# Optimization experiments

Hardware: AMD Instinct MI355X
Metric: run time of the kernel (lower is better)

Reference implementation:

```python
import jax, jax.numpy as jnp
import numpy as np

DIM = 512
HEADS = 8
HEAD_DIM = DIM // HEADS
SCALE = HEAD_DIM ** -0.5
LN_EPS = 1e-5


def _layernorm(t, g, b):
    mu = jnp.mean(t, axis=-1, keepdims=True)
    var = jnp.mean(jnp.square(t - mu), axis=-1, keepdims=True)
    return (t - mu) * jax.lax.rsqrt(var + LN_EPS) * g + b


def setup_inputs() -> dict:
    key = jax.random.key(0)
    ks = jax.random.split(key, 8)
    B, C, H, W = 2, DIM, 48, 48
    s = 1.0 / np.sqrt(DIM)
    return {
        "x": jax.random.normal(ks[0], (B, C, H, W), jnp.float32),
        "y": jax.random.normal(ks[1], (B, C, H, W), jnp.float32),
        # linear weights stored [in, out]
        "k_w": jax.random.uniform(ks[2], (DIM, DIM), jnp.float32, -s, s),
        "k_b": jax.random.uniform(ks[3], (DIM,), jnp.float32, -s, s),
        "qv_w": jax.random.uniform(ks[4], (DIM, 2 * DIM), jnp.float32, -s, s),
        "qv_b": jax.random.uniform(ks[5], (2 * DIM,), jnp.float32, -s, s),
        "lnx_g": jnp.ones((DIM,), jnp.float32),
        "lnx_b": jnp.zeros((DIM,), jnp.float32),
        "lny_g": jnp.ones((DIM,), jnp.float32),
        "lny_b": jnp.zeros((DIM,), jnp.float32),
    }


def _split_qv(t, qv_w, qv_b):
    B, N, C = t.shape
    qv = (t @ qv_w + qv_b).reshape(B, N, 2, HEADS, HEAD_DIM)
    qv = jnp.transpose(qv, (2, 0, 3, 1, 4))  # [2, B, h, N, d]
    return qv[0], qv[1]


def _heads(t):
    B, N, C = t.shape
    return jnp.transpose(t.reshape(B, N, HEADS, HEAD_DIM), (0, 2, 1, 3))  # [B,h,N,d]


def reference(x, y, k_w, k_b, qv_w, qv_b, lnx_g, lnx_b, lny_g, lny_b):
    B, C = x.shape[0], x.shape[1]
    xf = _layernorm(jnp.transpose(x.reshape(B, C, -1), (0, 2, 1)), lnx_g, lnx_b)  # [B,N,C]
    yf = _layernorm(jnp.transpose(y.reshape(B, C, -1), (0, 2, 1)), lny_g, lny_b)
    N = xf.shape[1]

    y_q, y_v = _split_qv(yf, qv_w, qv_b)
    x_q, x_v = _split_qv(xf, qv_w, qv_b)
    y_k = _heads(yf @ k_w + k_b)
    x_k = _heads(xf @ k_w + k_b)

    # branch 1: softmax(x_q y_k^T) x_v  -> standard [B,N,C]
    a1 = jax.nn.softmax(jnp.einsum('bhnd,bhmd->bhnm', x_q, y_k) * SCALE, axis=-1)
    xo = jnp.einsum('bhnm,bhmd->bhnd', a1, x_v)
    xo = jnp.transpose(xo, (0, 2, 1, 3)).reshape(B, N, C)

    # branch 2: faithful reproduction of torch quirk (x_k kept a leading 1-dim,
    # so the output [1,B,h,N,d].transpose(1,2).reshape(B,N,C) scrambles layout)
    a2 = jax.nn.softmax(jnp.einsum('bhnd,bhmd->bhnm', y_q, x_k) * SCALE, axis=-1)
    yo = jnp.einsum('bhnm,bhmd->bhnd', a2, y_v)  # [B,h,N,d]
    yo = jnp.transpose(yo[None], (0, 2, 1, 3, 4)).reshape(B, N, C)

    return jnp.concatenate([xo, yo], axis=0)  # [2B, N, C]
```

## Files before the change

### kernel.cpp

```cpp
#include <hip/hip_runtime.h>

#define DIM 512
#define NTOK 2304
#define HEADS 8
#define HD 64
#define LN_EPS 1e-5f
#define BNC 2359296
#define QSC 0.18033688011112042f

typedef __attribute__((ext_vector_type(8))) short short8;
typedef __attribute__((ext_vector_type(4))) short sh4;
typedef __attribute__((ext_vector_type(4))) float f32x4;

__device__ __forceinline__ short f2bf(float f) {
    union { float f; unsigned u; } x; x.f = f;
    unsigned r = (x.u + 0x7fffu + ((x.u >> 16) & 1u)) >> 16;
    return (short)(r & 0xffffu);
}
__device__ __forceinline__ unsigned fbits(float f) {
    union { float f; unsigned u; } x; x.f = f; return x.u;
}
__device__ __forceinline__ void gl2lds(const short* g, short* l) {
    __builtin_amdgcn_global_load_lds(
        (const __attribute__((address_space(1))) unsigned int*)g,
        (__attribute__((address_space(3))) unsigned int*)l, 16, 0, 0);
}

__global__ void k_prep(const float* __restrict__ x, const float* __restrict__ y,
                       float* __restrict__ mu, float* __restrict__ rs,
                       const float* __restrict__ qv_w, const float* __restrict__ k_w,
                       const float* __restrict__ qv_b, const float* __restrict__ k_b,
                       short* __restrict__ Wt, float* __restrict__ bias) {
    __shared__ __align__(16) float tile[64][65];
    int bx = blockIdx.x, tid = threadIdx.x;
    if (bx < 36) {
        int id = bx * 256 + tid;
        int n = id % NTOK;
        int sb = id / NTOK;
        int s = sb >> 1, b = sb & 1;
        const float* src = (s ? y : x) + (size_t)b * DIM * NTOK + n;
        float sum = 0.f, sq = 0.f;
        for (int c = 0; c < DIM; c++) {
            float v = src[(size_t)c * NTOK];
            sum += v; sq += v * v;
        }
        float m = sum * (1.0f / DIM);
        float var = sq * (1.0f / DIM) - m * m;
        mu[id] = m;
        rs[id] = rsqrtf(var + LN_EPS);
        return;
    }
    int idx = bx - 36;
    int jt = idx % 24, ct = idx / 24;
    int j0 = jt * 64, c0 = ct * 64;
    if (ct == 0 && tid < 64) {
        int j = j0 + tid;
        bias[j] = (j < 1024) ? qv_b[j] : k_b[j - 1024];
    }
    for (int slot = tid; slot < 1024; slot += 256) {
        int r = slot >> 4, q = slot & 15;
        int c = c0 + r;
        float4 v;
        if (j0 < 1024) v = *(const float4*)(qv_w + (size_t)c * 1024 + j0 + q * 4);
        else           v = *(const float4*)(k_w  + (size_t)c * 512  + (j0 - 1024) + q * 4);
        tile[r][q*4+0] = v.x; tile[r][q*4+1] = v.y;
        tile[r][q*4+2] = v.z; tile[r][q*4+3] = v.w;
    }
    __syncthreads();
    int jr = tid >> 2, cg = tid & 3;
    short8 o0, o1;
    for (int i = 0; i < 8; i++) o0[i] = f2bf(tile[cg*16+i][jr]);
    for (int i = 0; i < 8; i++) o1[i] = f2bf(tile[cg*16+8+i][jr]);
    short* dst = Wt + (size_t)(j0 + jr) * DIM + c0 + cg * 16;
    *(short8*)dst = o0;
    *(short8*)(dst + 8) = o1;
}

__global__ void k_normT(const float* __restrict__ x, const float* __restrict__ y,
                        const float* __restrict__ mu, const float* __restrict__ rs,
                        const float* __restrict__ gx, const float* __restrict__ bx,
                        const float* __restrict__ gy, const float* __restrict__ by,
                        short* __restrict__ T) {
    __shared__ __align__(16) float tile[64][65];
    int nt = blockIdx.x, ct = blockIdx.y, sb = blockIdx.z;
    int s = sb >> 1, b = sb & 1;
    int n0 = nt * 64, c0 = ct * 64;
    const float* src = (s ? y : x) + (size_t)b * DIM * NTOK;
    int tid = threadIdx.x;
    for (int slot = tid; slot < 1024; slot += 256) {
        int r = slot >> 4, q = slot & 15;
        const float* p = src + (size_t)(c0 + r) * NTOK + n0 + q * 4;
        float4 v = *(const float4*)p;
        tile[r][q*4+0] = v.x; tile[r][q*4+1] = v.y;
        tile[r][q*4+2] = v.z; tile[r][q*4+3] = v.w;
    }
    __syncthreads();
    const float* g  = s ? gy : gx;
    const float* be = s ? by : bx;
    int nr = tid >> 2, cg = tid & 3;
    int n = n0 + nr;
    float m = mu[sb * NTOK + n], r_ = rs[sb * NTOK + n];
    short8 o0, o1;
    for (int i = 0; i < 8; i++) {
        int c = c0 + cg * 16 + i;
        o0[i] = f2bf((tile[cg*16+i][nr] - m) * r_ * g[c] + be[c]);
    }
    for (int i = 0; i < 8; i++) {
        int c = c0 + cg * 16 + 8 + i;
        o1[i] = f2bf((tile[cg*16+8+i][nr] - m) * r_ * g[c] + be[c]);
    }
    short* dst = T + ((size_t)sb * NTOK + n) * DIM + c0 + cg * 16;
    *(short8*)dst = o0;
    *(short8*)(dst + 8) = o1;
}

__global__ void __launch_bounds__(256)
k_gemm(const short* __restrict__ T, const short* __restrict__ Wt,
       const float* __restrict__ bias, short* __restrict__ QVK) {
    __shared__ __align__(16) short As[128 * 64];
    __shared__ __align__(16) short Bs[128 * 64];
    int n0 = blockIdx.x * 128, j0 = blockIdx.y * 128, sb = blockIdx.z;
    int tid = threadIdx.x;
    int w = tid >> 6, l = tid & 63;
    int wr = w >> 1, wc = w & 1;
    int lrow = l & 15, quad = l >> 4;
    int r_in = (l >> 3) & 7, cc = l & 7;
    int ch = cc ^ r_in;
    int sw0 = (quad ^ (lrow & 7)) * 8;
    const short* Ab = T + (size_t)sb * NTOK * DIM;
    f32x4 acc[4][4] = {};
    for (int kk = 0; kk < 8; kk++) {
        if (kk) __syncthreads();
        for (int inst = 0; inst < 4; inst++) {
            int R = w * 32 + inst * 8 + r_in;
            gl2lds(Ab + (size_t)(n0 + R) * 512 + kk * 64 + ch * 8,
                   &As[(w * 32 + inst * 8) * 64]);
            gl2lds(Wt + (size_t)(j0 + R) * 512 + kk * 64 + ch * 8,
                   &Bs[(w * 32 + inst * 8) * 64]);
        }
        __syncthreads();
        for (int c2 = 0; c2 < 2; c2++) {
            int off = c2 ? (sw0 ^ 32) : sw0;
            short8 af[4], bf[4];
            for (int i = 0; i < 4; i++)
                af[i] = *(const short8*)&As[(wr*64 + i*16 + lrow) * 64 + off];
            for (int j = 0; j < 4; j++)
                bf[j] = *(const short8*)&Bs[(wc*64 + j*16 + lrow) * 64 + off];
            for (int i = 0; i < 4; i++)
                for (int j = 0; j < 4; j++)
                    acc[i][j] = __builtin_amdgcn_mfma_f32_16x16x32_bf16(af[i], bf[j], acc[i][j], 0, 0, 0);
        }
    }
    for (int i = 0; i < 4; i++)
        for (int j = 0; j < 4; j++) {
            int jj = j0 + wc * 64 + j * 16 + lrow;
            float bv = bias[jj];
            float sc = (jj < 512) ? QSC : 1.0f;
            for (int reg = 0; reg < 4; reg++) {
                int n = n0 + wr * 64 + i * 16 + quad * 4 + reg;
                QVK[((size_t)sb * NTOK + n) * 1536 + jj] = f2bf((acc[i][j][reg] + bv) * sc);
            }
        }
}

__global__ void k_vtrans(const short* __restrict__ QVK, short* __restrict__ VT) {
    __shared__ short tile[64][65];
    int n0 = blockIdx.x * 64, j0 = blockIdx.y * 64, sb = blockIdx.z;
    int tid = threadIdx.x;
    for (int slot = tid; slot < 512; slot += 256) {
        int r = slot >> 3, seg = slot & 7;
        short8 v = *(const short8*)(QVK + ((size_t)sb * NTOK + n0 + r) * 1536 + 512 + j0 + seg * 8);
        for (int i = 0; i < 8; i++) tile[r][seg * 8 + i] = v[i];
    }
    __syncthreads();
    int jr = tid >> 2, ng = tid & 3;
    short8 o0, o1;
    for (int i = 0; i < 8; i++) o0[i] = tile[ng*16+i][jr];
    for (int i = 0; i < 8; i++) o1[i] = tile[ng*16+8+i][jr];
    short* dst = VT + ((size_t)sb * 512 + j0 + jr) * NTOK + n0 + ng * 16;
    *(short8*)dst = o0;
    *(short8*)(dst + 8) = o1;
}

__global__ void __launch_bounds__(256)
k_attn(const short* __restrict__ QVK, const short* __restrict__ VT,
       float* __restrict__ out) {
    __shared__ __align__(16) short Ks[64 * 64];
    __shared__ __align__(16) short Vs[64 * 64];
    __shared__ __align__(16) short Qs[64 * 64];
    int qt = blockIdx.x;
    int yb = blockIdx.y;
    int br = yb >> 4;
    int b  = (yb >> 3) & 1;
    int h  = yb & 7;
    int tid = threadIdx.x;
    int w = tid >> 6, l = tid & 63;
    int lrow = l & 15, quad = l >> 4;
    int r_in = (l >> 3) & 7, cc = l & 7;
    int ch = cc ^ r_in;
    int sw0 = (quad ^ (lrow & 7)) * 8;
    int n0 = qt * 64;
    const short* Qg = QVK + ((size_t)(br * 2 + b) * NTOK) * 1536 + h * 64;
    const short* Kg = QVK + ((size_t)((1 - br) * 2 + b) * NTOK) * 1536 + 1024 + h * 64;
    const short* Vg = VT + ((size_t)(br * 2 + b) * 512 + h * 64) * NTOK;

    for (int inst = 0; inst < 2; inst++) {
        int R = w * 16 + inst * 8 + r_in;
        gl2lds(Qg + (size_t)(n0 + R) * 1536 + ch * 8, &Qs[(w * 16 + inst * 8) * 64]);
    }
    __syncthreads();
    short8 bq0 = *(const short8*)&Qs[(w * 16 + lrow) * 64 + sw0];
    short8 bq1 = *(const short8*)&Qs[(w * 16 + lrow) * 64 + (sw0 ^ 32)];
    short* Pw = &Qs[w * 16 * 64];

    short8 ones;
    for (int i = 0; i < 8; i++) ones[i] = (short)0x3F80;

    f32x4 Oacc[4] = {};
    f32x4 lacc = {};

    for (int mt = 0; mt < 36; mt++) {
        int m0 = mt * 64;
        __syncthreads();
        for (int inst = 0; inst < 2; inst++) {
            int R = w * 16 + inst * 8 + r_in;
            int Rb = (w * 16 + inst * 8) * 64;
            gl2lds(Kg + (size_t)(m0 + R) * 1536 + ch * 8, &Ks[Rb]);
            gl2lds(Vg + (size_t)R * NTOK + m0 + ch * 8, &Vs[Rb]);
        }
        __syncthreads();

        for (int sub = 0; sub < 4; sub++) {
            short8 ak0 = *(const short8*)&Ks[(sub * 16 + lrow) * 64 + sw0];
            short8 ak1 = *(const short8*)&Ks[(sub * 16 + lrow) * 64 + (sw0 ^ 32)];
            f32x4 a = {};
            a = __builtin_amdgcn_mfma_f32_16x16x32_bf16(ak0, bq0, a, 0, 0, 0);
            a = __builtin_amdgcn_mfma_f32_16x16x32_bf16(ak1, bq1, a, 0, 0, 0);
            float p0 = exp2f(a[0]), p1 = exp2f(a[1]);
            float p2 = exp2f(a[2]), p3 = exp2f(a[3]);
            uint2 pk;
            pk.x = __builtin_amdgcn_perm(fbits(p1), fbits(p0), 0x07060302u);
            pk.y = __builtin_amdgcn_perm(fbits(p3), fbits(p2), 0x07060302u);
            *(uint2*)&Pw[lrow * 64 + (((2 * sub + (quad >> 1)) ^ (lrow & 7)) * 8) + (quad & 1) * 4] = pk;
        }

        short8 ap0 = *(const short8*)&Pw[lrow * 64 + sw0];
        short8 ap1 = *(const short8*)&Pw[lrow * 64 + (sw0 ^ 32)];
        lacc = __builtin_amdgcn_mfma_f32_16x16x32_bf16(ones, ap0, lacc, 0, 0, 0);
        lacc = __builtin_amdgcn_mfma_f32_16x16x32_bf16(ones, ap1, lacc, 0, 0, 0);
        for (int ddt = 0; ddt < 4; ddt++) {
            short8 av0 = *(const short8*)&Vs[(ddt * 16 + lrow) * 64 + sw0];
            short8 av1 = *(const short8*)&Vs[(ddt * 16 + lrow) * 64 + (sw0 ^ 32)];
            Oacc[ddt] = __builtin_amdgcn_mfma_f32_16x16x32_bf16(av0, ap0, Oacc[ddt], 0, 0, 0);
            Oacc[ddt] = __builtin_amdgcn_mfma_f32_16x16x32_bf16(av1, ap1, Oacc[ddt], 0, 0, 0);
        }
    }

    float linv = 1.f / lacc[0];
    int n = n0 + w * 16 + lrow;
    for (int ddt = 0; ddt < 4; ddt++) {
        float4 o;
        o.x = Oacc[ddt][0] * linv;
        o.y = Oacc[ddt][1] * linv;
        o.z = Oacc[ddt][2] * linv;
        o.w = Oacc[ddt][3] * linv;
        if (br == 0)
            *(float4*)&out[((size_t)b * NTOK + n) * 512 + h * 64 + ddt * 16 + quad * 4] = o;
        else
            *(float4*)&out[(size_t)BNC + ((size_t)(h * 2 + b) * NTOK + n) * 64 + ddt * 16 + quad * 4] = o;
    }
}

extern "C" void kernel_launch(void* const* d_in, const int* in_sizes, int n_in,
                              void* d_out, int out_size, void* d_ws, size_t ws_size,
                              hipStream_t stream) {
    const float* x     = (const float*)d_in[0];
    const float* y     = (const float*)d_in[1];
    const float* k_w   = (const float*)d_in[2];
    const float* k_b   = (const float*)d_in[3];
    const float* qv_w  = (const float*)d_in[4];
    const float* qv_b  = (const float*)d_in[5];
    const float* lnx_g = (const float*)d_in[6];
    const float* lnx_b = (const float*)d_in[7];
    const float* lny_g = (const float*)d_in[8];
    const float* lny_b = (const float*)d_in[9];
    float* out = (float*)d_out;

    char* ws = (char*)d_ws;
    float* mu   = (float*)ws;
    float* rs   = mu + 9216;
    float* bias = rs + 9216;
    short* T    = (short*)(ws + 79872);
    short* Wt   = T + 4718592;
    short* QVK  = Wt + 786432;
    short* VT   = QVK + 14155776;

    k_prep  <<<228, 256, 0, stream>>>(x, y, mu, rs, qv_w, k_w, qv_b, k_b, Wt, bias);
    k_normT <<<dim3(36, 8, 4), 256, 0, stream>>>(x, y, mu, rs,
                                                 lnx_g, lnx_b, lny_g, lny_b, T);
    k_gemm  <<<dim3(18, 12, 4), 256, 0, stream>>>(T, Wt, bias, QVK);
    k_vtrans<<<dim3(36, 8, 4), 256, 0, stream>>>(QVK, VT);
    k_attn  <<<dim3(36, 32), 256, 0, stream>>>(QVK, VT, out);
}
```

Baseline: 234.1 us.

## Fuse V transpose into GEMM epilogue and parallelize LayerNorm statistics

The GEMM blocks that produce the V columns now stage their bf16 results in a swizzled LDS tile and write V already transposed, so the separate k_vtrans kernel and its extra pass over global memory go away. The LayerNorm statistics pass is split across four channel partitions per block and combined in shared memory, raising the stats block count from 36 to 144 so more CUs are busy. The V tiles are no longer written to QVK, and the V-tile GEMM blocks pay an extra LDS round trip and barrier in their epilogue.

```diff
diff --git a/kernel.cpp b/kernel.cpp
--- a/kernel.cpp
+++ b/kernel.cpp
@@ -32,25 +32,32 @@
                        const float* __restrict__ qv_b, const float* __restrict__ k_b,
                        short* __restrict__ Wt, float* __restrict__ bias) {
     __shared__ __align__(16) float tile[64][65];
+    __shared__ float pS[4][64], pQ[4][64];
     int bx = blockIdx.x, tid = threadIdx.x;
-    if (bx < 36) {
-        int id = bx * 256 + tid;
-        int n = id % NTOK;
-        int sb = id / NTOK;
+    if (bx < 144) {
+        int nt = bx % 36, sb = bx / 36;
+        int nl = tid & 63, part = tid >> 6;
+        int n = nt * 64 + nl;
         int s = sb >> 1, b = sb & 1;
         const float* src = (s ? y : x) + (size_t)b * DIM * NTOK + n;
         float sum = 0.f, sq = 0.f;
-        for (int c = 0; c < DIM; c++) {
+        for (int c = part * 128; c < part * 128 + 128; c++) {
             float v = src[(size_t)c * NTOK];
             sum += v; sq += v * v;
         }
-        float m = sum * (1.0f / DIM);
-        float var = sq * (1.0f / DIM) - m * m;
-        mu[id] = m;
-        rs[id] = rsqrtf(var + LN_EPS);
+        pS[part][nl] = sum; pQ[part][nl] = sq;
+        __syncthreads();
+        if (tid < 64) {
+            float ts = pS[0][tid] + pS[1][tid] + pS[2][tid] + pS[3][tid];
+            float tq = pQ[0][tid] + pQ[1][tid] + pQ[2][tid] + pQ[3][tid];
+            float m = ts * (1.0f / DIM);
+            float var = tq * (1.0f / DIM) - m * m;
+            mu[sb * NTOK + nt * 64 + tid] = m;
+            rs[sb * NTOK + nt * 64 + tid] = rsqrtf(var + LN_EPS);
+        }
         return;
     }
-    int idx = bx - 36;
+    int idx = bx - 144;
     int jt = idx % 24, ct = idx / 24;
     int j0 = jt * 64, c0 = ct * 64;
     if (ct == 0 && tid < 64) {
@@ -116,9 +123,11 @@
 
 __global__ void __launch_bounds__(256)
 k_gemm(const short* __restrict__ T, const short* __restrict__ Wt,
-       const float* __restrict__ bias, short* __restrict__ QVK) {
-    __shared__ __align__(16) short As[128 * 64];
-    __shared__ __align__(16) short Bs[128 * 64];
+       const float* __restrict__ bias, short* __restrict__ QVK,
+       short* __restrict__ VT) {
+    __shared__ __align__(16) short smem[2 * 128 * 64];
+    short* As = smem;
+    short* Bs = smem + 128 * 64;
     int n0 = blockIdx.x * 128, j0 = blockIdx.y * 128, sb = blockIdx.z;
     int tid = threadIdx.x;
     int w = tid >> 6, l = tid & 63;
@@ -151,35 +160,36 @@
                     acc[i][j] = __builtin_amdgcn_mfma_f32_16x16x32_bf16(af[i], bf[j], acc[i][j], 0, 0, 0);
         }
     }
-    for (int i = 0; i < 4; i++)
-        for (int j = 0; j < 4; j++) {
-            int jj = j0 + wc * 64 + j * 16 + lrow;
-            float bv = bias[jj];
-            float sc = (jj < 512) ? QSC : 1.0f;
-            for (int reg = 0; reg < 4; reg++) {
-                int n = n0 + wr * 64 + i * 16 + quad * 4 + reg;
-                QVK[((size_t)sb * NTOK + n) * 1536 + jj] = f2bf((acc[i][j][reg] + bv) * sc);
+    if (j0 >= 512 && j0 < 1024) {
+        __syncthreads();
+        for (int i = 0; i < 4; i++)
+            for (int j = 0; j < 4; j++) {
+                int jloc = wc * 64 + j * 16 + lrow;
+                float bv = bias[j0 + jloc];
+                int nloc = wr * 64 + i * 16 + quad * 4;
+                int c8 = nloc >> 3, half = (nloc >> 2) & 1;
+                sh4 pk;
+                for (int reg = 0; reg < 4; reg++) pk[reg] = f2bf(acc[i][j][reg] + bv);
+                *(sh4*)&smem[jloc * 128 + ((c8 ^ (jloc & 15)) * 8) + half * 4] = pk;
             }
-        }
-}
-
-__global__ void k_vtrans(const short* __restrict__ QVK, short* __restrict__ VT) {
-    __shared__ short tile[64][65];
-    int n0 = blockIdx.x * 64, j0 = blockIdx.y * 64, sb = blockIdx.z;
-    int tid = threadIdx.x;
-    for (int slot = tid; slot < 512; slot += 256) {
-        int r = slot >> 3, seg = slot & 7;
-        short8 v = *(const short8*)(QVK + ((size_t)sb * NTOK + n0 + r) * 1536 + 512 + j0 + seg * 8);
-        for (int i = 0; i < 8; i++) tile[r][seg * 8 + i] = v[i];
-    }
-    __syncthreads();
-    int jr = tid >> 2, ng = tid & 3;
-    short8 o0, o1;
-    for (int i = 0; i < 8; i++) o0[i] = tile[ng*16+i][jr];
-    for (int i = 0; i < 8; i++) o1[i] = tile[ng*16+8+i][jr];
-    short* dst = VT + ((size_t)sb * 512 + j0 + jr) * NTOK + n0 + ng * 16;
-    *(short8*)dst = o0;
-    *(short8*)(dst + 8) = o1;
+        __syncthreads();
+        for (int slot = tid; slot < 2048; slot += 256) {
+            int row = slot >> 4, seg = slot & 15;
+            short8 v = *(const short8*)&smem[row * 128 + ((seg ^ (row & 15)) * 8)];
+            *(short8*)(VT + ((size_t)sb * 512 + (j0 - 512) + row) * NTOK + n0 + seg * 8) = v;
+        }
+    } else {
+        for (int i = 0; i < 4; i++)
+            for (int j = 0; j < 4; j++) {
+                int jj = j0 + wc * 64 + j * 16 + lrow;
+                float bv = bias[jj];
+                float sc = (jj < 512) ? QSC : 1.0f;
+                for (int reg = 0; reg < 4; reg++) {
+                    int n = n0 + wr * 64 + i * 16 + quad * 4 + reg;
+                    QVK[((size_t)sb * NTOK + n) * 1536 + jj] = f2bf((acc[i][j][reg] + bv) * sc);
+                }
+            }
+    }
 }
 
 __global__ void __launch_bounds__(256)
@@ -295,10 +305,9 @@
     short* QVK  = Wt + 786432;
     short* VT   = QVK + 14155776;
 
-    k_prep  <<<228, 256, 0, stream>>>(x, y, mu, rs, qv_w, k_w, qv_b, k_b, Wt, bias);
+    k_prep  <<<336, 256, 0, stream>>>(x, y, mu, rs, qv_w, k_w, qv_b, k_b, Wt, bias);
     k_normT <<<dim3(36, 8, 4), 256, 0, stream>>>(x, y, mu, rs,
                                                  lnx_g, lnx_b, lny_g, lny_b, T);
-    k_gemm  <<<dim3(18, 12, 4), 256, 0, stream>>>(T, Wt, bias, QVK);
-    k_vtrans<<<dim3(36, 8, 4), 256, 0, stream>>>(QVK, VT);
+    k_gemm  <<<dim3(18, 12, 4), 256, 0, stream>>>(T, Wt, bias, QVK, VT);
     k_attn  <<<dim3(36, 32), 256, 0, stream>>>(QVK, VT, out);
 }
```

Result: faster. 205.6 us (-12.2%).
